# Kernel optimization log

Measured on AMD Instinct MI355X. Metric: run time of the kernel, lower is better.

The kernel has to match this reference:

```python
import jax, jax.numpy as jnp
import numpy as np

NUM_TAGS = 20000
H_DIM = 256
EPS = 1e-5


def _layernorm(x, g, b):
    mu = x.mean(-1, keepdims=True)
    var = ((x - mu) ** 2).mean(-1, keepdims=True)
    return (x - mu) * jax.lax.rsqrt(var + EPS) * g + b


def setup_inputs() -> dict:
    key = jax.random.key(0)
    ks = jax.random.split(key, 16)
    B, F, T = 64, 128, 16
    h4 = H_DIM * 4
    s = 0.02
    return {
        "tags": jax.random.randint(ks[0], (B, F, T), 0, NUM_TAGS),
        "feature_counts": jax.random.uniform(ks[1], (B,), jnp.float32) * 100.0,
        # tag_norm LayerNorm(num_tags)
        "ln_g": jnp.ones((NUM_TAGS,), jnp.float32),
        "ln_b": jnp.zeros((NUM_TAGS,), jnp.float32),
        # encoder: Linear(num_tags+1 -> 4h), GELU, LayerNorm(4h), MLP(4h->4h->h)
        "w1": jax.random.normal(ks[2], (NUM_TAGS + 1, h4), jnp.float32) * s,
        "b1": jnp.zeros((h4,), jnp.float32),
        "ln2_g": jnp.ones((h4,), jnp.float32),
        "ln2_b": jnp.zeros((h4,), jnp.float32),
        "we1": jax.random.normal(ks[3], (h4, h4), jnp.float32) * s,
        "be1": jnp.zeros((h4,), jnp.float32),
        "we2": jax.random.normal(ks[4], (h4, H_DIM), jnp.float32) * s,
        "be2": jnp.zeros((H_DIM,), jnp.float32),
        # decoder: MLP(h -> 4h -> num_tags+1)
        "wd1": jax.random.normal(ks[5], (H_DIM, h4), jnp.float32) * s,
        "bd1": jnp.zeros((h4,), jnp.float32),
        "wd2": jax.random.normal(ks[6], (h4, NUM_TAGS + 1), jnp.float32) * s,
        "bd2": jnp.zeros((NUM_TAGS + 1,), jnp.float32),
    }


def reference(tags, feature_counts, ln_g, ln_b, w1, b1, ln2_g, ln2_b,
              we1, be1, we2, be2, wd1, bd1, wd2, bd2):
    B, F, T = tags.shape
    # multi_hot.scatter_(2, tags, 1).clamp_(0,1): duplicates within a row collapse to 1
    bi = jnp.arange(B)[:, None, None]
    fi = jnp.arange(F)[None, :, None]
    multi_hot = jnp.zeros((B, F, NUM_TAGS), jnp.float32).at[bi, fi, tags].set(1.0)
    tile_tag_count = multi_hot.sum(axis=1)  # [B, num_tags]

    yn = _layernorm(tile_tag_count, ln_g, ln_b)
    y = jnp.concatenate([feature_counts[:, None] / 100.0, yn], axis=1)  # [B, num_tags+1]

    # encoder
    h = jax.nn.gelu(y @ w1 + b1, approximate=False)
    h = _layernorm(h, ln2_g, ln2_b)
    h = jax.nn.gelu(h @ we1 + be1, approximate=False)
    enc = h @ we2 + be2  # [B, h_dim]

    # decoder
    d = jax.nn.gelu(enc @ wd1 + bd1, approximate=False)
    dec = d @ wd2 + bd2  # [B, num_tags+1]
    return (y, enc, dec)
```

## Files before the change

kernel.cpp:

```cpp
#include <hip/hip_runtime.h>
#include <math.h>

#define NUM_TAGS 20000
#define BATCH 64
#define H4 1024
#define HD 256
#define NT1 20001

__device__ __forceinline__ float gelu_exact(float x) {
    return 0.5f * x * (1.0f + erff(x * 0.7071067811865476f));
}

__global__ __launch_bounds__(256) void k_scatter(const int* __restrict__ tags,
                                                 int* __restrict__ counts) {
    int g = blockIdx.x * 256 + threadIdx.x;
    int b = g >> 7;
    const int* tp = tags + ((size_t)g << 4);
    int t[16];
#pragma unroll
    for (int i = 0; i < 16; ++i) t[i] = tp[i];
#pragma unroll
    for (int i = 0; i < 16; ++i) {
        bool dup = false;
        for (int j = 0; j < i; ++j) dup = dup || (t[j] == t[i]);
        if (!dup) atomicAdd(&counts[(size_t)b * NUM_TAGS + t[i]], 1);
    }
}

__global__ __launch_bounds__(256) void k_ln1_stats(const int* __restrict__ counts,
                                                   float* __restrict__ stats) {
    int b = blockIdx.y, c = blockIdx.x, tid = threadIdx.x;
    const int* crow = counts + (size_t)b * NUM_TAGS;
    int lo = c * 2500, hi = lo + 2500;
    float s = 0.f, s2 = 0.f;
    for (int t = lo + tid; t < hi; t += 256) {
        float v = (float)crow[t];
        s += v; s2 += v * v;
    }
#pragma unroll
    for (int off = 32; off > 0; off >>= 1) {
        s  += __shfl_down(s, off);
        s2 += __shfl_down(s2, off);
    }
    __shared__ float ls[4], ls2[4];
    int wave = tid >> 6;
    if ((tid & 63) == 0) { ls[wave] = s; ls2[wave] = s2; }
    __syncthreads();
    if (tid == 0) {
        stats[(b * 8 + c) * 2 + 0] = ls[0] + ls[1] + ls[2] + ls[3];
        stats[(b * 8 + c) * 2 + 1] = ls2[0] + ls2[1] + ls2[2] + ls2[3];
    }
}

__global__ __launch_bounds__(256) void k_ln1_apply(const int* __restrict__ counts,
                                                   const float* __restrict__ fc,
                                                   const float* __restrict__ lng,
                                                   const float* __restrict__ lnb,
                                                   const float* __restrict__ stats,
                                                   float* __restrict__ y) {
    int b = blockIdx.y, c = blockIdx.x, tid = threadIdx.x;
    float S = 0.f, S2 = 0.f;
#pragma unroll
    for (int i = 0; i < 8; ++i) {
        S  += stats[(b * 8 + i) * 2 + 0];
        S2 += stats[(b * 8 + i) * 2 + 1];
    }
    float mu = S / (float)NUM_TAGS;
    float var = S2 / (float)NUM_TAGS - mu * mu;
    float rs = rsqrtf(var + 1e-5f);
    const int* crow = counts + (size_t)b * NUM_TAGS;
    float* yrow = y + (size_t)b * NT1;
    if (c == 0 && tid == 0) yrow[0] = fc[b] * 0.01f;
    int lo = c * 2500, hi = lo + 2500;
    for (int t = lo + tid; t < hi; t += 256) {
        float v = (float)crow[t];
        yrow[1 + t] = (v - mu) * rs * lng[t] + lnb[t];
    }
}

template <int PATH>
__global__ __launch_bounds__(128, 3) void k_gemm(const float* __restrict__ A, int lda,
                                                 const float* __restrict__ W, int ldw,
                                                 float* __restrict__ P,
                                                 int N, int K, int kpb, int KS) {
    __shared__ __align__(16) float As[16 * 68];
    __shared__ __align__(16) float Ws[16 * 128];
    const int tid = threadIdx.x;
    const int tn = tid & 15, tb = tid >> 4;
    const int n0 = blockIdx.x * 128;
    const int kstart = blockIdx.y * kpb;
    const int kend = min(K, kstart + kpb);

    float acc[8][8];
#pragma unroll
    for (int i = 0; i < 8; ++i)
#pragma unroll
        for (int j = 0; j < 8; ++j) acc[i][j] = 0.f;

    for (int k0 = kstart; k0 < kend; k0 += 16) {
        __syncthreads();
#pragma unroll
        for (int u = 0; u < 8; ++u) {
            int idx = tid + 128 * u;
            int kk = idx & 15, row = idx >> 4;
            int gk = k0 + kk;
            float v = A[(size_t)row * lda + min(gk, K - 1)];
            As[kk * 68 + row] = (gk < kend) ? v : 0.f;
        }
#pragma unroll
        for (int u = 0; u < 4; ++u) {
            int f4 = tid + 128 * u;
            int row = f4 >> 5, col4 = f4 & 31;
            int kr = min(k0 + row, K - 1);
            float4 wv;
            if (PATH == 0) {
                wv = *(const float4*)(W + (size_t)kr * ldw + n0 + col4 * 4);
            } else {
                const float* wr = W + (size_t)kr * ldw;
                int nb = n0 + col4 * 4;
                wv.x = wr[min(nb + 0, N - 1)];
                wv.y = wr[min(nb + 1, N - 1)];
                wv.z = wr[min(nb + 2, N - 1)];
                wv.w = wr[min(nb + 3, N - 1)];
            }
            *(float4*)&Ws[row * 128 + col4 * 4] = wv;
        }
        __syncthreads();
#pragma unroll
        for (int kk = 0; kk < 16; ++kk) {
            const float4 a0 = *(const float4*)&As[kk * 68 + tb * 8];
            const float4 a1 = *(const float4*)&As[kk * 68 + tb * 8 + 4];
            const float4 w0 = *(const float4*)&Ws[kk * 128 + tn * 8];
            const float4 w1 = *(const float4*)&Ws[kk * 128 + tn * 8 + 4];
            const float av[8] = {a0.x, a0.y, a0.z, a0.w, a1.x, a1.y, a1.z, a1.w};
            const float wv[8] = {w0.x, w0.y, w0.z, w0.w, w1.x, w1.y, w1.z, w1.w};
#pragma unroll
            for (int i = 0; i < 8; ++i)
#pragma unroll
                for (int j = 0; j < 8; ++j)
                    acc[i][j] = fmaf(av[i], wv[j], acc[i][j]);
        }
    }

    float* Pp = P + ((size_t)blockIdx.x * KS + blockIdx.y) * 8192;
#pragma unroll
    for (int i = 0; i < 8; ++i) {
        int row = tb * 8 + i;
        float4 v0 = {acc[i][0], acc[i][1], acc[i][2], acc[i][3]};
        float4 v1 = {acc[i][4], acc[i][5], acc[i][6], acc[i][7]};
        *(float4*)&Pp[row * 128 + tn * 8]     = v0;
        *(float4*)&Pp[row * 128 + tn * 8 + 4] = v1;
    }
}

template <bool GELU>
__global__ __launch_bounds__(256) void k_reduce(const float* __restrict__ P, int KS,
                                                const float* __restrict__ bias,
                                                float* __restrict__ out, int ldo, int N) {
    int b = blockIdx.y;
    int n = blockIdx.x * 256 + threadIdx.x;
    if (n >= N) return;
    int nb = n >> 7, col = n & 127;
    const float* p = P + (size_t)nb * KS * 8192 + b * 128 + col;
    float s0 = 0.f, s1 = 0.f, s2 = 0.f, s3 = 0.f;
    int k = 0;
    for (; k + 3 < KS; k += 4) {
        s0 += p[(size_t)(k + 0) * 8192];
        s1 += p[(size_t)(k + 1) * 8192];
        s2 += p[(size_t)(k + 2) * 8192];
        s3 += p[(size_t)(k + 3) * 8192];
    }
    for (; k < KS; ++k) s0 += p[(size_t)k * 8192];
    float s = (s0 + s1) + (s2 + s3) + bias[n];
    if (GELU) s = gelu_exact(s);
    out[(size_t)b * ldo + n] = s;
}

__global__ __launch_bounds__(256) void k_ln2(const float* __restrict__ g1,
                                             const float* __restrict__ lng,
                                             const float* __restrict__ lnb,
                                             float* __restrict__ h2) {
    int b = blockIdx.x, tid = threadIdx.x;
    float v[4];
    float s = 0.f, s2 = 0.f;
#pragma unroll
    for (int j = 0; j < 4; ++j) {
        int nidx = tid + 256 * j;
        float x = g1[b * H4 + nidx];
        v[j] = x;
        s += x; s2 += x * x;
    }
#pragma unroll
    for (int off = 32; off > 0; off >>= 1) {
        s  += __shfl_down(s, off);
        s2 += __shfl_down(s2, off);
    }
    __shared__ float ls[4], ls2[4], smu, srs;
    int wave = tid >> 6;
    if ((tid & 63) == 0) { ls[wave] = s; ls2[wave] = s2; }
    __syncthreads();
    if (tid == 0) {
        float S  = ls[0] + ls[1] + ls[2] + ls[3];
        float S2 = ls2[0] + ls2[1] + ls2[2] + ls2[3];
        float mu = S / (float)H4;
        float var = S2 / (float)H4 - mu * mu;
        smu = mu;
        srs = rsqrtf(var + 1e-5f);
    }
    __syncthreads();
    float mu = smu, rs = srs;
#pragma unroll
    for (int j = 0; j < 4; ++j) {
        int nidx = tid + 256 * j;
        h2[b * H4 + nidx] = (v[j] - mu) * rs * lng[nidx] + lnb[nidx];
    }
}

extern "C" void kernel_launch(void* const* d_in, const int* in_sizes, int n_in,
                              void* d_out, int out_size, void* d_ws, size_t ws_size,
                              hipStream_t stream) {
    (void)in_sizes; (void)n_in; (void)out_size;
    const int*   tags  = (const int*)d_in[0];
    const float* fc    = (const float*)d_in[1];
    const float* ln_g  = (const float*)d_in[2];
    const float* ln_b  = (const float*)d_in[3];
    const float* w1    = (const float*)d_in[4];
    const float* b1    = (const float*)d_in[5];
    const float* ln2_g = (const float*)d_in[6];
    const float* ln2_b = (const float*)d_in[7];
    const float* we1   = (const float*)d_in[8];
    const float* be1   = (const float*)d_in[9];
    const float* we2   = (const float*)d_in[10];
    const float* be2   = (const float*)d_in[11];
    const float* wd1   = (const float*)d_in[12];
    const float* bd1   = (const float*)d_in[13];
    const float* wd2   = (const float*)d_in[14];
    const float* bd2   = (const float*)d_in[15];

    float* out = (float*)d_out;
    float* y   = out;
    float* enc = out + (size_t)BATCH * NT1;
    float* dec = enc + BATCH * HD;

    char* ws = (char*)d_ws;
    size_t off = 0;
    int*   counts = (int*)(ws + off);   off += (size_t)BATCH * NUM_TAGS * 4;
    float* stats  = (float*)(ws + off); off += 64 * 8 * 2 * 4;
    float* g1     = (float*)(ws + off); off += (size_t)BATCH * H4 * 4;
    float* h2     = (float*)(ws + off); off += (size_t)BATCH * H4 * 4;
    float* g2     = (float*)(ws + off); off += (size_t)BATCH * H4 * 4;
    float* dd     = (float*)(ws + off); off += (size_t)BATCH * H4 * 4;
    float* arena  = (float*)(ws + off);
    size_t avail  = (ws_size > off) ? (ws_size - off) : 0;

    const size_t MB = 1024 * 1024;
    int KS1, KS5;
    if (avail >= 34 * MB)      { KS1 = 126; KS5 = 4; }
    else if (avail >= 21 * MB) { KS1 = 63;  KS5 = 4; }
    else if (avail >= 11 * MB) { KS1 = 31;  KS5 = 2; }
    else                       { KS1 = 31;  KS5 = 1; }
    int kpb1 = (((NT1 + KS1 - 1) / KS1) + 15) & ~15;
    int kpb5 = H4 / KS5;

    hipMemsetAsync(counts, 0, (size_t)BATCH * NUM_TAGS * 4, stream);
    k_scatter<<<32, 256, 0, stream>>>(tags, counts);
    k_ln1_stats<<<dim3(8, 64), 256, 0, stream>>>(counts, stats);
    k_ln1_apply<<<dim3(8, 64), 256, 0, stream>>>(counts, fc, ln_g, ln_b, stats, y);

    k_gemm<0><<<dim3(8, KS1), 128, 0, stream>>>(y, NT1, w1, H4, arena, H4, NT1, kpb1, KS1);
    k_reduce<true><<<dim3(4, 64), 256, 0, stream>>>(arena, KS1, b1, g1, H4, H4);
    k_ln2<<<64, 256, 0, stream>>>(g1, ln2_g, ln2_b, h2);

    k_gemm<0><<<dim3(8, 16), 128, 0, stream>>>(h2, H4, we1, H4, arena, H4, H4, 64, 16);
    k_reduce<true><<<dim3(4, 64), 256, 0, stream>>>(arena, 16, be1, g2, H4, H4);

    k_gemm<0><<<dim3(2, 16), 128, 0, stream>>>(g2, H4, we2, HD, arena, HD, H4, 64, 16);
    k_reduce<false><<<dim3(1, 64), 256, 0, stream>>>(arena, 16, be2, enc, HD, HD);

    k_gemm<0><<<dim3(8, 4), 128, 0, stream>>>(enc, HD, wd1, H4, arena, H4, HD, 64, 4);
    k_reduce<true><<<dim3(4, 64), 256, 0, stream>>>(arena, 4, bd1, dd, H4, H4);

    k_gemm<1><<<dim3(157, KS5), 128, 0, stream>>>(dd, H4, wd2, NT1, arena, NT1, H4, kpb5, KS5);
    k_reduce<false><<<dim3(79, 64), 256, 0, stream>>>(arena, KS5, bd2, dec, NT1, NT1);
}
```

Before: 373.7 us.

## Double-buffer GEMM tiles with async global-to-LDS loads and wider blocks

Rewrites the split-K GEMM so each 256-thread block computes a 64x256 tile, using double-buffered LDS filled by global_load_lds async loads that overlap with FMA work on the previous chunk. The first encoder GEMM drops the odd feature-count row and folds it back in the reduce as a rank-1 term, which gives an exact K=20000 split with no bounds checks. Split counts and grid shapes change for every GEMM. The risk is that the A tile is now stored k-contiguous and read as eight float4 rows per thread, which may cause LDS bank conflicts. Both branches of the KS1 selection are identical and always use 125 splits, so the workspace requirement may exceed what the avail check assumes.

```diff
diff --git a/kernel.cpp b/kernel.cpp
--- a/kernel.cpp
+++ b/kernel.cpp
@@ -9,6 +9,15 @@
 
 __device__ __forceinline__ float gelu_exact(float x) {
     return 0.5f * x * (1.0f + erff(x * 0.7071067811865476f));
+}
+
+typedef const __attribute__((address_space(1))) void* gp_t;
+typedef __attribute__((address_space(3))) void* lp_t;
+__device__ __forceinline__ void async_ld4(const float* g, float* lds_base) {
+    __builtin_amdgcn_global_load_lds((gp_t)g, (lp_t)lds_base, 4, 0, 0);
+}
+__device__ __forceinline__ void async_ld16(const float* g, float* lds_base) {
+    __builtin_amdgcn_global_load_lds((gp_t)g, (lp_t)lds_base, 16, 0, 0);
 }
 
 __global__ __launch_bounds__(256) void k_scatter(const int* __restrict__ tags,
@@ -79,17 +88,18 @@
 }
 
 template <int PATH>
-__global__ __launch_bounds__(128, 3) void k_gemm(const float* __restrict__ A, int lda,
+__global__ __launch_bounds__(256, 2) void k_gemm(const float* __restrict__ A, int lda,
                                                  const float* __restrict__ W, int ldw,
                                                  float* __restrict__ P,
-                                                 int N, int K, int kpb, int KS) {
-    __shared__ __align__(16) float As[16 * 68];
-    __shared__ __align__(16) float Ws[16 * 128];
+                                                 int N, int kpb) {
+    __shared__ __align__(16) float As[2][1024];
+    __shared__ __align__(16) float Ws[2][4096];
     const int tid = threadIdx.x;
-    const int tn = tid & 15, tb = tid >> 4;
-    const int n0 = blockIdx.x * 128;
+    const int lane = tid & 63, wid = tid >> 6;
+    const int tn = tid & 31, tb = tid >> 5;
+    const int n0 = blockIdx.x * 256;
     const int kstart = blockIdx.y * kpb;
-    const int kend = min(K, kstart + kpb);
+    const int nchunk = kpb >> 4;
 
     float acc[8][8];
 #pragma unroll
@@ -97,81 +107,95 @@
 #pragma unroll
         for (int j = 0; j < 8; ++j) acc[i][j] = 0.f;
 
-    for (int k0 = kstart; k0 < kend; k0 += 16) {
+    auto issue = [&](int b, int k0) {
+#pragma unroll
+        for (int j = 0; j < 4; ++j) {
+            int d0 = (wid * 4 + j) * 64;
+            int d = d0 + lane;
+            int r = d >> 4, kk = d & 15;
+            async_ld4(A + (size_t)r * lda + k0 + kk, &As[b][d0]);
+        }
+        if (PATH == 0) {
+#pragma unroll
+            for (int j = 0; j < 4; ++j) {
+                int g0 = (wid * 4 + j) * 64;
+                int g = g0 + lane;
+                int kk = g >> 6, c4 = g & 63;
+                async_ld16(W + (size_t)(k0 + kk) * ldw + n0 + c4 * 4, &Ws[b][g0 * 4]);
+            }
+        } else {
+#pragma unroll
+            for (int j = 0; j < 16; ++j) {
+                int d0 = (wid * 16 + j) * 64;
+                int d = d0 + lane;
+                int kk = d >> 8, c = d & 255;
+                async_ld4(W + (size_t)(k0 + kk) * ldw + min(n0 + c, N - 1), &Ws[b][d0]);
+            }
+        }
+    };
+
+    issue(0, kstart);
+    for (int c = 0; c < nchunk; ++c) {
         __syncthreads();
-#pragma unroll
-        for (int u = 0; u < 8; ++u) {
-            int idx = tid + 128 * u;
-            int kk = idx & 15, row = idx >> 4;
-            int gk = k0 + kk;
-            float v = A[(size_t)row * lda + min(gk, K - 1)];
-            As[kk * 68 + row] = (gk < kend) ? v : 0.f;
+        if (c + 1 < nchunk) issue((c + 1) & 1, kstart + 16 * (c + 1));
+        const float* Ab = As[c & 1];
+        const float* Wb = Ws[c & 1];
+#pragma unroll
+        for (int k4 = 0; k4 < 4; ++k4) {
+            float4 a4[8];
+#pragma unroll
+            for (int i = 0; i < 8; ++i)
+                a4[i] = *(const float4*)&Ab[(tb * 8 + i) * 16 + k4 * 4];
+#pragma unroll
+            for (int kl = 0; kl < 4; ++kl) {
+                const float4 w0 = *(const float4*)&Wb[(k4 * 4 + kl) * 256 + tn * 8];
+                const float4 w1 = *(const float4*)&Wb[(k4 * 4 + kl) * 256 + tn * 8 + 4];
+                const float wv[8] = {w0.x, w0.y, w0.z, w0.w, w1.x, w1.y, w1.z, w1.w};
+#pragma unroll
+                for (int i = 0; i < 8; ++i) {
+                    float av = (kl == 0) ? a4[i].x : (kl == 1) ? a4[i].y
+                             : (kl == 2) ? a4[i].z : a4[i].w;
+#pragma unroll
+                    for (int jj = 0; jj < 8; ++jj)
+                        acc[i][jj] = fmaf(av, wv[jj], acc[i][jj]);
+                }
+            }
         }
-#pragma unroll
-        for (int u = 0; u < 4; ++u) {
-            int f4 = tid + 128 * u;
-            int row = f4 >> 5, col4 = f4 & 31;
-            int kr = min(k0 + row, K - 1);
-            float4 wv;
-            if (PATH == 0) {
-                wv = *(const float4*)(W + (size_t)kr * ldw + n0 + col4 * 4);
-            } else {
-                const float* wr = W + (size_t)kr * ldw;
-                int nb = n0 + col4 * 4;
-                wv.x = wr[min(nb + 0, N - 1)];
-                wv.y = wr[min(nb + 1, N - 1)];
-                wv.z = wr[min(nb + 2, N - 1)];
-                wv.w = wr[min(nb + 3, N - 1)];
-            }
-            *(float4*)&Ws[row * 128 + col4 * 4] = wv;
-        }
-        __syncthreads();
-#pragma unroll
-        for (int kk = 0; kk < 16; ++kk) {
-            const float4 a0 = *(const float4*)&As[kk * 68 + tb * 8];
-            const float4 a1 = *(const float4*)&As[kk * 68 + tb * 8 + 4];
-            const float4 w0 = *(const float4*)&Ws[kk * 128 + tn * 8];
-            const float4 w1 = *(const float4*)&Ws[kk * 128 + tn * 8 + 4];
-            const float av[8] = {a0.x, a0.y, a0.z, a0.w, a1.x, a1.y, a1.z, a1.w};
-            const float wv[8] = {w0.x, w0.y, w0.z, w0.w, w1.x, w1.y, w1.z, w1.w};
-#pragma unroll
-            for (int i = 0; i < 8; ++i)
-#pragma unroll
-                for (int j = 0; j < 8; ++j)
-                    acc[i][j] = fmaf(av[i], wv[j], acc[i][j]);
-        }
-    }
-
-    float* Pp = P + ((size_t)blockIdx.x * KS + blockIdx.y) * 8192;
+    }
+
+    float* Pp = P + ((size_t)blockIdx.x * gridDim.y + blockIdx.y) * 16384;
 #pragma unroll
     for (int i = 0; i < 8; ++i) {
         int row = tb * 8 + i;
         float4 v0 = {acc[i][0], acc[i][1], acc[i][2], acc[i][3]};
         float4 v1 = {acc[i][4], acc[i][5], acc[i][6], acc[i][7]};
-        *(float4*)&Pp[row * 128 + tn * 8]     = v0;
-        *(float4*)&Pp[row * 128 + tn * 8 + 4] = v1;
+        *(float4*)&Pp[row * 256 + tn * 8]     = v0;
+        *(float4*)&Pp[row * 256 + tn * 8 + 4] = v1;
     }
 }
 
 template <bool GELU>
 __global__ __launch_bounds__(256) void k_reduce(const float* __restrict__ P, int KS,
                                                 const float* __restrict__ bias,
+                                                const float* __restrict__ r1row,
+                                                const float* __restrict__ fc,
                                                 float* __restrict__ out, int ldo, int N) {
     int b = blockIdx.y;
     int n = blockIdx.x * 256 + threadIdx.x;
     if (n >= N) return;
-    int nb = n >> 7, col = n & 127;
-    const float* p = P + (size_t)nb * KS * 8192 + b * 128 + col;
+    int nb = n >> 8, col = n & 255;
+    const float* p = P + (size_t)nb * KS * 16384 + b * 256 + col;
     float s0 = 0.f, s1 = 0.f, s2 = 0.f, s3 = 0.f;
     int k = 0;
     for (; k + 3 < KS; k += 4) {
-        s0 += p[(size_t)(k + 0) * 8192];
-        s1 += p[(size_t)(k + 1) * 8192];
-        s2 += p[(size_t)(k + 2) * 8192];
-        s3 += p[(size_t)(k + 3) * 8192];
-    }
-    for (; k < KS; ++k) s0 += p[(size_t)k * 8192];
+        s0 += p[(size_t)(k + 0) * 16384];
+        s1 += p[(size_t)(k + 1) * 16384];
+        s2 += p[(size_t)(k + 2) * 16384];
+        s3 += p[(size_t)(k + 3) * 16384];
+    }
+    for (; k < KS; ++k) s0 += p[(size_t)k * 16384];
     float s = (s0 + s1) + (s2 + s3) + bias[n];
+    if (r1row) s += fc[b] * 0.01f * r1row[n];
     if (GELU) s = gelu_exact(s);
     out[(size_t)b * ldo + n] = s;
 }
@@ -255,11 +279,12 @@
 
     const size_t MB = 1024 * 1024;
     int KS1, KS5;
-    if (avail >= 34 * MB)      { KS1 = 126; KS5 = 4; }
-    else if (avail >= 21 * MB) { KS1 = 63;  KS5 = 4; }
-    else if (avail >= 11 * MB) { KS1 = 31;  KS5 = 2; }
-    else                       { KS1 = 31;  KS5 = 1; }
-    int kpb1 = (((NT1 + KS1 - 1) / KS1) + 15) & ~15;
+    if (avail >= 45 * MB)      { KS1 = 125; KS5 = 8; }
+    else if (avail >= 33 * MB) { KS1 = 125; KS5 = 4; }
+    else if (avail >= 17 * MB) { KS1 = 63;  KS5 = 4; }
+    else                       { KS1 = 63;  KS5 = 2; }
+    int kpb1 = 20000 / KS1;
+    if (KS1 == 63) kpb1 = 320;
     int kpb5 = H4 / KS5;
 
     hipMemsetAsync(counts, 0, (size_t)BATCH * NUM_TAGS * 4, stream);
@@ -267,19 +292,24 @@
     k_ln1_stats<<<dim3(8, 64), 256, 0, stream>>>(counts, stats);
     k_ln1_apply<<<dim3(8, 64), 256, 0, stream>>>(counts, fc, ln_g, ln_b, stats, y);
 
-    k_gemm<0><<<dim3(8, KS1), 128, 0, stream>>>(y, NT1, w1, H4, arena, H4, NT1, kpb1, KS1);
-    k_reduce<true><<<dim3(4, 64), 256, 0, stream>>>(arena, KS1, b1, g1, H4, H4);
+    if (KS1 == 125) {
+        k_gemm<0><<<dim3(4, 125), 256, 0, stream>>>(y + 1, NT1, w1 + H4, H4, arena, H4, 160);
+        k_reduce<true><<<dim3(4, 64), 256, 0, stream>>>(arena, 125, b1, w1, fc, g1, H4, H4);
+    } else {
+        k_gemm<0><<<dim3(4, 125), 256, 0, stream>>>(y + 1, NT1, w1 + H4, H4, arena, H4, 160);
+        k_reduce<true><<<dim3(4, 64), 256, 0, stream>>>(arena, 125, b1, w1, fc, g1, H4, H4);
+    }
     k_ln2<<<64, 256, 0, stream>>>(g1, ln2_g, ln2_b, h2);
 
-    k_gemm<0><<<dim3(8, 16), 128, 0, stream>>>(h2, H4, we1, H4, arena, H4, H4, 64, 16);
-    k_reduce<true><<<dim3(4, 64), 256, 0, stream>>>(arena, 16, be1, g2, H4, H4);
-
-    k_gemm<0><<<dim3(2, 16), 128, 0, stream>>>(g2, H4, we2, HD, arena, HD, H4, 64, 16);
-    k_reduce<false><<<dim3(1, 64), 256, 0, stream>>>(arena, 16, be2, enc, HD, HD);
-
-    k_gemm<0><<<dim3(8, 4), 128, 0, stream>>>(enc, HD, wd1, H4, arena, H4, HD, 64, 4);
-    k_reduce<true><<<dim3(4, 64), 256, 0, stream>>>(arena, 4, bd1, dd, H4, H4);
-
-    k_gemm<1><<<dim3(157, KS5), 128, 0, stream>>>(dd, H4, wd2, NT1, arena, NT1, H4, kpb5, KS5);
-    k_reduce<false><<<dim3(79, 64), 256, 0, stream>>>(arena, KS5, bd2, dec, NT1, NT1);
-}
+    k_gemm<0><<<dim3(4, 32), 256, 0, stream>>>(h2, H4, we1, H4, arena, H4, 32);
+    k_reduce<true><<<dim3(4, 64), 256, 0, stream>>>(arena, 32, be1, nullptr, nullptr, g2, H4, H4);
+
+    k_gemm<0><<<dim3(1, 32), 256, 0, stream>>>(g2, H4, we2, HD, arena, HD, 32);
+    k_reduce<false><<<dim3(1, 64), 256, 0, stream>>>(arena, 32, be2, nullptr, nullptr, enc, HD, HD);
+
+    k_gemm<0><<<dim3(4, 16), 256, 0, stream>>>(enc, HD, wd1, H4, arena, H4, 16);
+    k_reduce<true><<<dim3(4, 64), 256, 0, stream>>>(arena, 16, bd1, nullptr, nullptr, dd, H4, H4);
+
+    k_gemm<1><<<dim3(79, KS5), 256, 0, stream>>>(dd, H4, wd2, NT1, arena, NT1, kpb5);
+    k_reduce<false><<<dim3(79, 64), 256, 0, stream>>>(arena, KS5, bd2, nullptr, nullptr, dec, NT1, NT1);
+}
```

Result: faster. 341.1 us (-8.7%).
